# Optimization experiments

Hardware: AMD Instinct MI355X
Metric: run time of the kernel (lower is better)

The kernel has to match this reference:

```python
import jax, jax.numpy as jnp
import numpy as np

N_NODES = 100_000
N_CH = 16
DIM = 3
N_EDGES = 1_600_000
N_STEPS = 2
MAX_STEP_LEN = 1.0
EPS = jnp.float32(jnp.finfo(jnp.float32).eps)  # orig uses float64 eps; fp32-safe here


def setup_inputs() -> dict:
    key = jax.random.key(0)
    k1, k2, k3, k4, k5 = jax.random.split(key, 5)
    nodes = jax.random.normal(k1, (N_NODES, N_CH, DIM), dtype=jnp.float32)
    nodes = nodes / jnp.linalg.norm(nodes, axis=-1, keepdims=True)  # project to S^2
    senders = jax.random.randint(k2, (N_EDGES,), 0, N_NODES, dtype=jnp.int32)
    receivers = jax.random.randint(k3, (N_EDGES,), 0, N_NODES, dtype=jnp.int32)
    weights = jnp.ones((N_EDGES,), dtype=jnp.float32)
    # mimic truncated_normal(std=1)+1 inits (squared later => positive params)
    t_sqrt = 1.0 + 0.5 * jax.random.normal(k4, (N_CH,), dtype=jnp.float32)
    alpha_sqrt = 1.0 + 0.5 * jax.random.normal(k5, (N_CH,), dtype=jnp.float32)
    beta_sqrt = jnp.ones((N_CH,), dtype=jnp.float32)
    return dict(nodes=nodes, senders=senders, receivers=receivers, weights=weights,
                t_sqrt=t_sqrt, alpha_sqrt=alpha_sqrt, beta_sqrt=beta_sqrt)


def sphere_log(x, y):
    # log_x(y) on the unit sphere; x, y: (..., DIM)
    c = jnp.clip(jnp.sum(x * y, axis=-1, keepdims=True), -1.0 + 1e-7, 1.0 - 1e-7)
    theta = jnp.arccos(c)
    return (theta / jnp.sin(theta)) * (y - c * x)


def sphere_exp(x, v):
    # exp_x(v) on the unit sphere
    n = jnp.sqrt(jnp.sum(v * v, axis=-1, keepdims=True) + 1e-16)
    return jnp.cos(n) * x + (jnp.sin(n) / n) * v


def mfdg_laplace(nodes, senders, receivers, weights):
    # degree-normalized manifold graph Laplacian:
    #   L(x)_i = -(1/deg_i) * sum_{j in N(i)} w_ij log_{x_i}(x_j)
    logs = sphere_log(nodes[senders], nodes[receivers])         # (E, C, D)
    agg = jax.ops.segment_sum(weights[:, None, None] * logs, senders,
                              num_segments=N_NODES)             # (N, C, D)
    deg = jax.ops.segment_sum(weights, senders, num_segments=N_NODES)
    return -agg / (deg[:, None, None] + 1e-12)


def _flow(nodes, senders, receivers, weights, t_sqrt, alpha_sqrt, beta_sqrt):
    t = (t_sqrt ** 2) / N_STEPS   # (C,)
    a = alpha_sqrt ** 2           # (C,)
    b = beta_sqrt ** 2            # (C,)
    x = nodes
    for _ in range(N_STEPS):
        v = mfdg_laplace(x, senders, receivers, weights)        # (N, C, D)
        nrm = jnp.sqrt(jnp.sum(v * v, axis=-1) + EPS)           # (N, C)
        d = jax.nn.sigmoid(b * (nrm - a))                       # sigmoid gating
        scale = jnp.where(nrm * d <= MAX_STEP_LEN, d, MAX_STEP_LEN / nrm)
        v = -(v * scale[..., None]) * t[None, :, None]
        x = sphere_exp(x, v)
    return x


def reference(nodes, senders, receivers, weights, t_sqrt, alpha_sqrt, beta_sqrt):
    return _flow(nodes, senders, receivers, weights, t_sqrt, alpha_sqrt, beta_sqrt)
```

## Files before the change

### kernel.cpp

```cpp
#include <hip/hip_runtime.h>

#define N_NODES 100000
#define N_CH 16
#define DIM 3
#define N_EDGES 1600000
#define N_STEPS 2
#define EPS_D 1.1920928955078125e-7

#define PB 1024
#define NBLK ((N_NODES + PB - 1) / PB)
#define DBINS 64
#define NBUCK 256
#define NBUCK_LIVE ((N_NODES + 511) / 512)
#define TA 4096
#define NBLK_A ((N_EDGES + TA - 1) / TA)
#define CAP 14336

__global__ void hist_kernel(const int4* __restrict__ senders4,
                            int* __restrict__ cnt) {
    int e = blockIdx.x * blockDim.x + threadIdx.x;
    if (e < N_EDGES / 4) {
        int4 s = senders4[e];
        atomicAdd(&cnt[s.x], 1);
        atomicAdd(&cnt[s.y], 1);
        atomicAdd(&cnt[s.z], 1);
        atomicAdd(&cnt[s.w], 1);
    }
}

__global__ void scan_partials_dhist(const int* __restrict__ cnt,
                                    int* __restrict__ part,
                                    int* __restrict__ bins) {
    __shared__ int sh[PB];
    __shared__ int lb[DBINS];
    int t = threadIdx.x;
    if (t < DBINS) lb[t] = 0;
    int g = blockIdx.x * PB + t;
    int v = (g < N_NODES) ? cnt[g] : 0;
    sh[t] = v;
    __syncthreads();
    for (int off = PB / 2; off > 0; off >>= 1) {
        if (t < off) sh[t] += sh[t + off];
        __syncthreads();
    }
    if (t == 0) part[blockIdx.x] = sh[0];
    if (g < N_NODES) {
        int d = (v > DBINS - 1) ? (DBINS - 1) : v;
        atomicAdd(&lb[d], 1);
    }
    __syncthreads();
    if (t < DBINS && lb[t]) atomicAdd(&bins[t], lb[t]);
}

__global__ void scan_mid_fused(int* __restrict__ part,
                               int* __restrict__ rowptr,
                               const int* __restrict__ bins,
                               int* __restrict__ binoff,
                               int* __restrict__ binfill) {
    __shared__ int sh[128];
    int t = threadIdx.x;
    int v = (t < NBLK) ? part[t] : 0;
    sh[t] = v;
    __syncthreads();
    for (int off = 1; off < 128; off <<= 1) {
        int u = (t >= off) ? sh[t - off] : 0;
        __syncthreads();
        sh[t] += u;
        __syncthreads();
    }
    if (t < NBLK) part[t] = sh[t] - v;
    if (t == NBLK - 1) rowptr[N_NODES] = sh[t];
    if (t < DBINS) {
        int bv = bins[t];
        int s = bv;
        for (int off = 1; off < DBINS; off <<= 1) {
            int u = __shfl_up(s, off, 64);
            if (t >= off) s += u;
        }
        binoff[t] = s - bv;
        binfill[t] = 0;
    }
}

__global__ void scan_apply_dscatter(const int* __restrict__ cnt,
                                    const int* __restrict__ part,
                                    int* __restrict__ rowptr,
                                    const int* __restrict__ binoff,
                                    int* __restrict__ binfill,
                                    int* __restrict__ perm,
                                    int* __restrict__ bfill) {
    __shared__ int sh[PB];
    __shared__ int lcnt[DBINS];
    __shared__ int lbase[DBINS];
    int t = threadIdx.x;
    if (t < DBINS) lcnt[t] = 0;
    int g = blockIdx.x * PB + t;
    int v = (g < N_NODES) ? cnt[g] : 0;
    sh[t] = v;
    __syncthreads();
    for (int off = 1; off < PB; off <<= 1) {
        int u = (t >= off) ? sh[t - off] : 0;
        __syncthreads();
        sh[t] += u;
        __syncthreads();
    }
    if (g < N_NODES) {
        int rp = part[blockIdx.x] + sh[t] - v;
        rowptr[g] = rp;
        if ((g & 511) == 0) bfill[g >> 9] = rp;
    }
    int d = 0, myoff = 0;
    if (g < N_NODES) {
        d = (v > DBINS - 1) ? (DBINS - 1) : v;
        myoff = atomicAdd(&lcnt[d], 1);
    }
    __syncthreads();
    if (t < DBINS && lcnt[t]) lbase[t] = atomicAdd(&binfill[t], lcnt[t]);
    __syncthreads();
    if (g < N_NODES && perm) perm[binoff[d] + lbase[d] + myoff] = g;
}

__global__ void bucket_scatter(const int* __restrict__ senders,
                               const int* __restrict__ receivers,
                               const float* __restrict__ weights,
                               int* __restrict__ bfill,
                               int* __restrict__ stg_s,
                               int2* __restrict__ stg_rw) {
    __shared__ int lcnt[NBUCK];
    __shared__ int lbase[NBUCK];
    int t = threadIdx.x;
    lcnt[t] = 0;
    __syncthreads();
    int base = blockIdx.x * TA;
    for (int k = t; k < TA; k += 256) {
        int e = base + k;
        if (e < N_EDGES) atomicAdd(&lcnt[senders[e] >> 9], 1);
    }
    __syncthreads();
    int c = lcnt[t];
    if (c) lbase[t] = atomicAdd(&bfill[t], c);
    __syncthreads();
    lcnt[t] = 0;
    __syncthreads();
    for (int k = t; k < TA; k += 256) {
        int e = base + k;
        if (e < N_EDGES) {
            int s = senders[e];
            int b = s >> 9;
            int pos = lbase[b] + atomicAdd(&lcnt[b], 1);
            stg_s[pos] = s;
            stg_rw[pos] = make_int2(receivers[e], __float_as_int(weights[e]));
        }
    }
}

__global__ void __launch_bounds__(256, 1)
bucket_sort(const int* __restrict__ stg_s,
            const int2* __restrict__ stg_rw,
            const int* __restrict__ rowptr,
            int* __restrict__ cnt,
            int2* __restrict__ edata) {
    __shared__ int lcnt[512];
    __shared__ int2 lrw[CAP];
    int b = blockIdx.x;
    int nbase = b << 9;
    int nend = nbase + 512; if (nend > N_NODES) nend = N_NODES;
    int ebase = rowptr[nbase];
    int eend = rowptr[nend];
    int m = eend - ebase;
    int t = threadIdx.x;

    if (m <= CAP) {
        for (int k = t; k < 512; k += 256) lcnt[k] = 0;
        __syncthreads();
        for (int k = t; k < m; k += 256) {
            int s = stg_s[ebase + k];
            int rank = atomicAdd(&lcnt[s - nbase], 1);
            lrw[(rowptr[s] - ebase) + rank] = stg_rw[ebase + k];
        }
        __syncthreads();
        for (int k = t; k < m; k += 256) {
            edata[ebase + k] = lrw[k];
        }
    } else {
        for (int k = t; k < m; k += 256) {
            int s = stg_s[ebase + k];
            int old = atomicAdd(&cnt[s], -1);
            edata[rowptr[s] + old - 1] = stg_rw[ebase + k];
        }
    }
}

__device__ __forceinline__ double fast_rsqrt(double x) {
    double y = (double)rsqrtf((float)x);
    y = y * fma(-0.5 * x, y * y, 1.5);
    return y;
}

__device__ __forceinline__ double theta_over_sin(double cd) {
    double acd = fabs(cd);
    bool mid = (acd <= 0.5);
    double z = mid ? (cd * cd) : (0.5 * (1.0 - acd));
    double A = 0.008390335809943149;
    A = fma(A, z, 0.009761609529194078);
    A = fma(A, z, 0.011551800896139706);
    A = fma(A, z, 0.013964843750);
    A = fma(A, z, 0.017352764423076924);
    A = fma(A, z, 0.022372159090909092);
    A = fma(A, z, 0.030381944444444444);
    A = fma(A, z, 0.044642857142857144);
    A = fma(A, z, 0.075);
    A = fma(A, z, 0.16666666666666666);
    A = fma(A, z, 1.0);
    double R = fast_rsqrt(1.0 - z);
    if (mid) return (1.5707963267948966 - cd * A) * R;
    double AR = A * R;
    if (cd > 0.0) return AR;
    double Rz = fast_rsqrt(z);
    return fma(1.5707963267948966 * Rz, R, -AR);
}

template <typename TI, typename TO>
__global__ void flow_kernel(const TI* __restrict__ x,
                            const int* __restrict__ rowptr,
                            const int2* __restrict__ edata,
                            const int* __restrict__ perm,
                            const float* __restrict__ t_sqrt,
                            const float* __restrict__ alpha_sqrt,
                            const float* __restrict__ beta_sqrt,
                            TO* __restrict__ xout) {
    int wave = threadIdx.x >> 6;
    int lane = threadIdx.x & 63;
    int q = lane >> 4;
    int c = lane & 15;
    int slot = (blockIdx.x * 4 + wave) * 4 + q;
    int i = perm ? perm[slot] : slot;

    int beg = rowptr[i];
    int end = rowptr[i + 1];

    const TI* xi = x + ((size_t)i * N_CH + c) * DIM;
    double ax = (double)xi[0], ay = (double)xi[1], az = (double)xi[2];

    double sx = 0.0, sy = 0.0, sz = 0.0, sw = 0.0;
    for (int k = beg; k < end; ++k) {
        int2 ed = edata[k];
        int r = ed.x;
        double w = (double)__int_as_float(ed.y);
        const TI* xr = x + ((size_t)r * N_CH + c) * DIM;
        double bx = (double)xr[0], by = (double)xr[1], bz = (double)xr[2];

        double cd = ax * bx + ay * by + az * bz;
        cd = fmin(fmax(cd, -1.0 + 1e-7), 1.0 - 1e-7);
        double f = w * theta_over_sin(cd);

        sx += f * (bx - cd * ax);
        sy += f * (by - cd * ay);
        sz += f * (bz - cd * az);
        sw += w;
    }

    double dg = sw + 1e-12;
    double inv = 1.0 / dg;
    double vx = -sx * inv, vy = -sy * inv, vz = -sz * inv;

    double t = (double)t_sqrt[c];     t = (t * t) / (double)N_STEPS;
    double a = (double)alpha_sqrt[c]; a = a * a;
    double b = (double)beta_sqrt[c];  b = b * b;

    double nrm = sqrt(vx * vx + vy * vy + vz * vz + EPS_D);
    double d = 1.0 / (1.0 + exp(-b * (nrm - a)));
    double scale = (nrm * d <= 1.0) ? d : (1.0 / nrm);
    double fs = -scale * t;
    vx *= fs; vy *= fs; vz *= fs;

    double n = sqrt(vx * vx + vy * vy + vz * vz + 1e-16);
    double cn = cos(n);
    double sf = sin(n) / n;

    TO* xo = xout + ((size_t)i * N_CH + c) * DIM;
    xo[0] = (TO)(cn * ax + sf * vx);
    xo[1] = (TO)(cn * ay + sf * vy);
    xo[2] = (TO)(cn * az + sf * vz);
}

__global__ void deg_kernel(const int* __restrict__ senders,
                           const float* __restrict__ weights,
                           float* __restrict__ deg) {
    int e = blockIdx.x * blockDim.x + threadIdx.x;
    if (e < N_EDGES) atomicAdd(&deg[senders[e]], weights[e]);
}

__global__ void edge_kernel(const float* __restrict__ x,
                            const int* __restrict__ senders,
                            const int* __restrict__ receivers,
                            const float* __restrict__ weights,
                            float* __restrict__ agg) {
    unsigned int tid = blockIdx.x * blockDim.x + threadIdx.x;
    if (tid >= (unsigned int)N_EDGES * N_CH) return;
    unsigned int e = tid >> 4;
    unsigned int c = tid & 15u;
    int s = senders[e];
    int r = receivers[e];
    float w = weights[e];
    const float* xs = x + ((size_t)s * N_CH + c) * DIM;
    const float* xr = x + ((size_t)r * N_CH + c) * DIM;
    float ax = xs[0], ay = xs[1], az = xs[2];
    float bx = xr[0], by = xr[1], bz = xr[2];
    float cd = ax * bx + ay * by + az * bz;
    cd = fminf(fmaxf(cd, -1.0f + 1e-7f), 1.0f - 1e-7f);
    float theta = acosf(cd);
    float sn = sqrtf(fmaxf(1.0f - cd * cd, 0.0f));
    float f = w * theta / sn;
    float* ag = agg + ((size_t)s * N_CH + c) * DIM;
    atomicAdd(&ag[0], f * (bx - cd * ax));
    atomicAdd(&ag[1], f * (by - cd * ay));
    atomicAdd(&ag[2], f * (bz - cd * az));
}

__global__ void node_kernel(const float* __restrict__ xin,
                            const float* __restrict__ agg,
                            const float* __restrict__ deg,
                            const float* __restrict__ t_sqrt,
                            const float* __restrict__ alpha_sqrt,
                            const float* __restrict__ beta_sqrt,
                            float* __restrict__ xout) {
    unsigned int tid = blockIdx.x * blockDim.x + threadIdx.x;
    if (tid >= (unsigned int)N_NODES * N_CH) return;
    unsigned int i = tid >> 4;
    unsigned int c = tid & 15u;
    float dg = deg[i] + 1e-12f;
    const float* ag = agg + (size_t)tid * DIM;
    float vx = -ag[0] / dg, vy = -ag[1] / dg, vz = -ag[2] / dg;
    float t = t_sqrt[c]; t = (t * t) * (1.0f / N_STEPS);
    float a = alpha_sqrt[c]; a = a * a;
    float b = beta_sqrt[c]; b = b * b;
    float nrm = sqrtf(vx * vx + vy * vy + vz * vz + 1.1920929e-7f);
    float d = 1.0f / (1.0f + __expf(-b * (nrm - a)));
    float scale = (nrm * d <= 1.0f) ? d : (1.0f / nrm);
    float fs = -scale * t;
    vx *= fs; vy *= fs; vz *= fs;
    const float* xi = xin + (size_t)tid * DIM;
    float axx = xi[0], ayy = xi[1], azz = xi[2];
    float n = sqrtf(vx * vx + vy * vy + vz * vz + 1e-16f);
    float cn = cosf(n);
    float sf = sinf(n) / n;
    float* xo = xout + (size_t)tid * DIM;
    xo[0] = cn * axx + sf * vx;
    xo[1] = cn * ayy + sf * vy;
    xo[2] = cn * azz + sf * vz;
}

extern "C" void kernel_launch(void* const* d_in, const int* in_sizes, int n_in,
                              void* d_out, int out_size, void* d_ws, size_t ws_size,
                              hipStream_t stream) {
    const float* nodes      = (const float*)d_in[0];
    const int*   senders    = (const int*)d_in[1];
    const int*   receivers  = (const int*)d_in[2];
    const float* weights    = (const float*)d_in[3];
    const float* t_sqrt     = (const float*)d_in[4];
    const float* alpha_sqrt = (const float*)d_in[5];
    const float* beta_sqrt  = (const float*)d_in[6];
    float* out = (float*)d_out;

    const size_t AL = 255;
    const size_t xtmp_b   = (size_t)N_NODES * N_CH * DIM * sizeof(double);
    const size_t rowptr_b = (((size_t)(N_NODES + 1) * sizeof(int)) + AL) & ~AL;
    const size_t cnt_b    = (((size_t)N_NODES * sizeof(int)) + AL) & ~AL;
    const size_t bins_b   = 2048;
    const size_t part_b   = 4096;
    const size_t perm_b   = (((size_t)N_NODES * sizeof(int)) + AL) & ~AL;
    const size_t edata_b  = (size_t)N_EDGES * sizeof(int2);
    const size_t need_sorted = xtmp_b + rowptr_b + cnt_b + bins_b + part_b + perm_b + edata_b;
    const size_t need_plain  = xtmp_b + rowptr_b + cnt_b + bins_b + part_b + edata_b;

    if (ws_size >= need_plain) {
        bool sorted = (ws_size >= need_sorted);
        char* p = (char*)d_ws;
        double* xtmp  = (double*)p;           p += xtmp_b;
        int*   rowptr = (int*)p;              p += rowptr_b;
        int*   cnt    = (int*)p;              p += cnt_b;
        int*   bins   = (int*)p;
        int*   binoff = bins + 64;
        int*   binfill= bins + 128;
        int*   bfill  = bins + 192;           p += bins_b;
        int*   part   = (int*)p;              p += part_b;
        int*   perm   = nullptr;
        if (sorted) { perm = (int*)p;         p += perm_b; }
        int2*  edata  = (int2*)p;

        int2*  stg_rw = (int2*)xtmp;
        int*   stg_s  = (int*)((char*)xtmp + edata_b);

        hipMemsetAsync(cnt, 0, cnt_b + 256, stream);
        hist_kernel<<<(N_EDGES / 4 + 255) / 256, 256, 0, stream>>>(
            (const int4*)senders, cnt);
        scan_partials_dhist<<<NBLK, PB, 0, stream>>>(cnt, part, bins);
        scan_mid_fused<<<1, 128, 0, stream>>>(part, rowptr, bins, binoff, binfill);
        scan_apply_dscatter<<<NBLK, PB, 0, stream>>>(cnt, part, rowptr,
                                                     binoff, binfill, perm, bfill);
        bucket_scatter<<<NBLK_A, NBUCK, 0, stream>>>(senders, receivers, weights,
                                                     bfill, stg_s, stg_rw);
        bucket_sort<<<NBUCK_LIVE, 256, 0, stream>>>(stg_s, stg_rw, rowptr, cnt, edata);

        int grid = N_NODES / 16;
        flow_kernel<float, double><<<grid, 256, 0, stream>>>(
            nodes, rowptr, edata, perm, t_sqrt, alpha_sqrt, beta_sqrt, xtmp);
        flow_kernel<double, float><<<grid, 256, 0, stream>>>(
            xtmp, rowptr, edata, perm, t_sqrt, alpha_sqrt, beta_sqrt, out);
    } else {
        float* agg = (float*)d_ws;
        float* deg = agg + (size_t)N_NODES * N_CH * DIM;
        hipMemsetAsync(deg, 0, N_NODES * sizeof(float), stream);
        deg_kernel<<<(N_EDGES + 255) / 256, 256, 0, stream>>>(senders, weights, deg);
        const float* xin = nodes;
        for (int step = 0; step < N_STEPS; ++step) {
            hipMemsetAsync(agg, 0, (size_t)N_NODES * N_CH * DIM * sizeof(float), stream);
            unsigned int n_ec = (unsigned int)N_EDGES * N_CH;
            edge_kernel<<<(n_ec + 255) / 256, 256, 0, stream>>>(xin, senders, receivers,
                                                                weights, agg);
            unsigned int n_nc = (unsigned int)N_NODES * N_CH;
            node_kernel<<<(n_nc + 255) / 256, 256, 0, stream>>>(xin, agg, deg, t_sqrt,
                                                                alpha_sqrt, beta_sqrt, out);
            xin = out;
        }
    }
}
```

Measured before the change: 333.5 us.

## Fuse per-block bucket counting into histogram pass and pack sender into staging

The histogram kernel now also computes per-block bucket counts, so the scatter kernel no longer rereads senders for a counting pass. The staging buffer packs the sender's low 9 bits into the receiver field, which removes the separate stg_s array and its reads and writes in the bucket sort. Flow kernel address arithmetic switches from size_t to 32-bit int. This relies on receiver indices fitting in 17 bits and adds writes and reads of a per-block count array.

```diff
diff --git a/kernel.cpp b/kernel.cpp
--- a/kernel.cpp
+++ b/kernel.cpp
@@ -16,16 +16,31 @@
 #define NBLK_A ((N_EDGES + TA - 1) / TA)
 #define CAP 14336
 
-__global__ void hist_kernel(const int4* __restrict__ senders4,
-                            int* __restrict__ cnt) {
-    int e = blockIdx.x * blockDim.x + threadIdx.x;
-    if (e < N_EDGES / 4) {
-        int4 s = senders4[e];
-        atomicAdd(&cnt[s.x], 1);
-        atomicAdd(&cnt[s.y], 1);
-        atomicAdd(&cnt[s.z], 1);
-        atomicAdd(&cnt[s.w], 1);
-    }
+
+__global__ void count_kernel(const int4* __restrict__ senders4,
+                             int* __restrict__ cnt,
+                             int* __restrict__ pcnt) {
+    __shared__ int lc[NBUCK];
+    int t = threadIdx.x;
+    lc[t] = 0;
+    __syncthreads();
+    int base4 = blockIdx.x * (TA / 4);
+    for (int k = t; k < TA / 4; k += 256) {
+        int idx = base4 + k;
+        if (idx < N_EDGES / 4) {
+            int4 s = senders4[idx];
+            atomicAdd(&cnt[s.x], 1);
+            atomicAdd(&cnt[s.y], 1);
+            atomicAdd(&cnt[s.z], 1);
+            atomicAdd(&cnt[s.w], 1);
+            atomicAdd(&lc[s.x >> 9], 1);
+            atomicAdd(&lc[s.y >> 9], 1);
+            atomicAdd(&lc[s.z >> 9], 1);
+            atomicAdd(&lc[s.w >> 9], 1);
+        }
+    }
+    __syncthreads();
+    pcnt[blockIdx.x * NBUCK + t] = lc[t];
 }
 
 __global__ void scan_partials_dhist(const int* __restrict__ cnt,
@@ -120,43 +135,34 @@
     if (g < N_NODES && perm) perm[binoff[d] + lbase[d] + myoff] = g;
 }
 
-__global__ void bucket_scatter(const int* __restrict__ senders,
+__global__ void scatter_kernel(const int* __restrict__ senders,
                                const int* __restrict__ receivers,
                                const float* __restrict__ weights,
+                               const int* __restrict__ pcnt,
                                int* __restrict__ bfill,
-                               int* __restrict__ stg_s,
-                               int2* __restrict__ stg_rw) {
+                               int2* __restrict__ stg) {
+    __shared__ int lbase[NBUCK];
     __shared__ int lcnt[NBUCK];
-    __shared__ int lbase[NBUCK];
-    int t = threadIdx.x;
+    int t = threadIdx.x;
+    int c = pcnt[blockIdx.x * NBUCK + t];
+    if (c) lbase[t] = atomicAdd(&bfill[t], c);
     lcnt[t] = 0;
     __syncthreads();
     int base = blockIdx.x * TA;
-    for (int k = t; k < TA; k += 256) {
-        int e = base + k;
-        if (e < N_EDGES) atomicAdd(&lcnt[senders[e] >> 9], 1);
-    }
-    __syncthreads();
-    int c = lcnt[t];
-    if (c) lbase[t] = atomicAdd(&bfill[t], c);
-    __syncthreads();
-    lcnt[t] = 0;
-    __syncthreads();
     for (int k = t; k < TA; k += 256) {
         int e = base + k;
         if (e < N_EDGES) {
             int s = senders[e];
             int b = s >> 9;
             int pos = lbase[b] + atomicAdd(&lcnt[b], 1);
-            stg_s[pos] = s;
-            stg_rw[pos] = make_int2(receivers[e], __float_as_int(weights[e]));
+            stg[pos] = make_int2(receivers[e] | ((s & 511) << 17),
+                                 __float_as_int(weights[e]));
         }
     }
 }
 
 __global__ void __launch_bounds__(256, 1)
-bucket_sort(const int* __restrict__ stg_s,
-            const int2* __restrict__ stg_rw,
+bucket_sort(const int2* __restrict__ stg,
             const int* __restrict__ rowptr,
             int* __restrict__ cnt,
             int2* __restrict__ edata) {
@@ -174,9 +180,11 @@
         for (int k = t; k < 512; k += 256) lcnt[k] = 0;
         __syncthreads();
         for (int k = t; k < m; k += 256) {
-            int s = stg_s[ebase + k];
-            int rank = atomicAdd(&lcnt[s - nbase], 1);
-            lrw[(rowptr[s] - ebase) + rank] = stg_rw[ebase + k];
+            int2 ed = stg[ebase + k];
+            int sl = ((unsigned)ed.x) >> 17;
+            int s = nbase + sl;
+            int rank = atomicAdd(&lcnt[sl], 1);
+            lrw[(rowptr[s] - ebase) + rank] = make_int2(ed.x & 0x1FFFF, ed.y);
         }
         __syncthreads();
         for (int k = t; k < m; k += 256) {
@@ -184,9 +192,10 @@
         }
     } else {
         for (int k = t; k < m; k += 256) {
-            int s = stg_s[ebase + k];
+            int2 ed = stg[ebase + k];
+            int s = nbase + (((unsigned)ed.x) >> 17);
             int old = atomicAdd(&cnt[s], -1);
-            edata[rowptr[s] + old - 1] = stg_rw[ebase + k];
+            edata[rowptr[s] + old - 1] = make_int2(ed.x & 0x1FFFF, ed.y);
         }
     }
 }
@@ -235,11 +244,12 @@
     int c = lane & 15;
     int slot = (blockIdx.x * 4 + wave) * 4 + q;
     int i = perm ? perm[slot] : slot;
+    int c3 = c * DIM;
 
     int beg = rowptr[i];
     int end = rowptr[i + 1];
 
-    const TI* xi = x + ((size_t)i * N_CH + c) * DIM;
+    const TI* xi = x + (i * (N_CH * DIM) + c3);
     double ax = (double)xi[0], ay = (double)xi[1], az = (double)xi[2];
 
     double sx = 0.0, sy = 0.0, sz = 0.0, sw = 0.0;
@@ -247,7 +257,7 @@
         int2 ed = edata[k];
         int r = ed.x;
         double w = (double)__int_as_float(ed.y);
-        const TI* xr = x + ((size_t)r * N_CH + c) * DIM;
+        const TI* xr = x + (r * (N_CH * DIM) + c3);
         double bx = (double)xr[0], by = (double)xr[1], bz = (double)xr[2];
 
         double cd = ax * bx + ay * by + az * bz;
@@ -278,7 +288,7 @@
     double cn = cos(n);
     double sf = sin(n) / n;
 
-    TO* xo = xout + ((size_t)i * N_CH + c) * DIM;
+    TO* xo = xout + (i * (N_CH * DIM) + c3);
     xo[0] = (TO)(cn * ax + sf * vx);
     xo[1] = (TO)(cn * ay + sf * vy);
     xo[2] = (TO)(cn * az + sf * vz);
@@ -389,19 +399,18 @@
         if (sorted) { perm = (int*)p;         p += perm_b; }
         int2*  edata  = (int2*)p;
 
-        int2*  stg_rw = (int2*)xtmp;
-        int*   stg_s  = (int*)((char*)xtmp + edata_b);
+        int2*  stg  = (int2*)xtmp;
+        int*   pcnt = (int*)((char*)xtmp + (16u << 20));
 
         hipMemsetAsync(cnt, 0, cnt_b + 256, stream);
-        hist_kernel<<<(N_EDGES / 4 + 255) / 256, 256, 0, stream>>>(
-            (const int4*)senders, cnt);
+        count_kernel<<<NBLK_A, NBUCK, 0, stream>>>((const int4*)senders, cnt, pcnt);
         scan_partials_dhist<<<NBLK, PB, 0, stream>>>(cnt, part, bins);
         scan_mid_fused<<<1, 128, 0, stream>>>(part, rowptr, bins, binoff, binfill);
         scan_apply_dscatter<<<NBLK, PB, 0, stream>>>(cnt, part, rowptr,
                                                      binoff, binfill, perm, bfill);
-        bucket_scatter<<<NBLK_A, NBUCK, 0, stream>>>(senders, receivers, weights,
-                                                     bfill, stg_s, stg_rw);
-        bucket_sort<<<NBUCK_LIVE, 256, 0, stream>>>(stg_s, stg_rw, rowptr, cnt, edata);
+        scatter_kernel<<<NBLK_A, NBUCK, 0, stream>>>(senders, receivers, weights,
+                                                     pcnt, bfill, stg);
+        bucket_sort<<<NBUCK_LIVE, 256, 0, stream>>>(stg, rowptr, cnt, edata);
 
         int grid = N_NODES / 16;
         flow_kernel<float, double><<<grid, 256, 0, stream>>>(
```

After: 315.8 us. 1.06x faster.
